# Performance work log

Measured on AMD Instinct MI355X. Metric: run time of the kernel, lower is better.

## Reference

```python
import jax, jax.numpy as jnp
import numpy as np

IGNORE_INDEX = -100


def setup_inputs() -> dict:
    key = jax.random.key(0)
    k1, k2, k3 = jax.random.split(key, 3)
    B, S, D, V = 2, 4096, 2048, 32000
    outputs = jax.random.normal(k1, (B, S, D), dtype=jnp.float32)
    # LM-head weight, nn.Linear convention: [vocab, embed_dim], scaled like typical init
    weight = jax.random.normal(k2, (V, D), dtype=jnp.float32) * (D ** -0.5)
    targets = jax.random.randint(k3, (B, S), 0, V, dtype=jnp.int64)
    return {"outputs": outputs, "weight": weight, "targets": targets}


def reference(outputs, weight, targets):
    # Flatten tokens: [B, S, D] -> [N, D], [B, S] -> [N]
    D = outputs.shape[-1]
    x = outputs.reshape(-1, D)            # [N, D]
    t = targets.reshape(-1)               # [N]
    # Fused linear projection: logits [N, V]
    logits = jnp.einsum("nd,vd->nv", x, weight)
    logp = jax.nn.log_softmax(logits, axis=-1)
    valid = t != IGNORE_INDEX
    safe_t = jnp.where(valid, t, 0)
    # Gather target log-prob per token
    nll = -jnp.take_along_axis(logp, safe_t[:, None], axis=1)[:, 0]  # [N]
    n_valid = jnp.maximum(jnp.sum(valid.astype(nll.dtype)), 1.0)
    loss = jnp.sum(jnp.where(valid, nll, 0.0)) / n_valid
    return loss
```

## Files before the change

kernel.cpp:

```cpp
#include <hip/hip_runtime.h>
#include <hip/hip_bf16.h>
#include <math.h>

#define IGNORE_INDEX (-100)

typedef __attribute__((ext_vector_type(4))) float f32x4;
typedef __attribute__((ext_vector_type(16))) float f32x16;
typedef __attribute__((ext_vector_type(4))) int i32x4;
typedef __attribute__((ext_vector_type(8))) int i32x8;

static const int NTOK = 2 * 4096;
static const int DIM  = 2048;
static const int VOC  = 32000;
static const int BM = 256, BN = 256;
static const int KS = 64;
static const int NPH = DIM / KS;
static const int NVT = VOC / BN;
static const int MT  = NTOK / BM;
static const float WSCALE = 16.0f;
#define SCL1 0x7F7F7F7F


__device__ inline void gload_lds16(const void* g, void* l) {
  __builtin_amdgcn_global_load_lds(
      (const __attribute__((address_space(1))) void*)g,
      (__attribute__((address_space(3))) void*)l,
      16, 0, 0);
}


__global__ void cast_f32_fp8(const float* __restrict__ in,
                             unsigned char* __restrict__ out, long n8, float scale) {
  long i0 = (long)blockIdx.x * blockDim.x + threadIdx.x;
  long stride = (long)gridDim.x * blockDim.x;
  for (long i = i0; i < n8; i += stride) {
    const float4* p = (const float4*)(in + i * 8);
    float4 a = p[0], b = p[1];
    int lo = __builtin_amdgcn_cvt_pk_fp8_f32(a.x * scale, a.y * scale, 0, false);
    lo = __builtin_amdgcn_cvt_pk_fp8_f32(a.z * scale, a.w * scale, lo, true);
    int hi = __builtin_amdgcn_cvt_pk_fp8_f32(b.x * scale, b.y * scale, 0, false);
    hi = __builtin_amdgcn_cvt_pk_fp8_f32(b.z * scale, b.w * scale, hi, true);
    int2 o; o.x = lo; o.y = hi;
    *(int2*)(out + i * 8) = o;
  }
}


#define VM8  asm volatile("s_waitcnt vmcnt(8)" ::: "memory")
#define VM4  asm volatile("s_waitcnt vmcnt(4)" ::: "memory")
#define VM0  asm volatile("s_waitcnt vmcnt(0)" ::: "memory")
#define BARRIER asm volatile("s_barrier" ::: "memory")
#define LGKM0 asm volatile("s_waitcnt lgkmcnt(0)" ::: "memory")

#define MS(ACC, AV, BV) \
  ACC = __builtin_amdgcn_mfma_scale_f32_32x32x64_f8f6f4( \
      AV, BV, ACC, 0, 0, 0, SCL1, 0, SCL1)

#define PACK8(LO, HI) {LO[0], LO[1], LO[2], LO[3], HI[0], HI[1], HI[2], HI[3]}

__launch_bounds__(512, 2)
__global__ void lce_gemm(const unsigned char* __restrict__ xq,
                         const unsigned char* __restrict__ wq,
                         float* __restrict__ pmax, float* __restrict__ psum) {
  extern __shared__ char smem[];
  char* smA = smem;
  char* smB = smem + 65536;

  const int nwg = NVT * MT;
  const int cpx = nwg >> 3;
  const int bid = blockIdx.x;
  const int swz = (bid & 7) * cpx + (bid >> 3);
  const int vt = swz / MT;
  const int mt = swz % MT;
  const int m0 = mt * BM;
  const int v0 = vt * BN;

  const int tid = threadIdx.x;
  const int lane = tid & 63;
  const int w = tid >> 6;
  const int wr = w >> 2, wc = w & 3;
  const int lc = lane & 31;
  const int lh = lane >> 5;

  f32x16 acc[4][2];
#pragma unroll
  for (int i = 0; i < 4; ++i)
#pragma unroll
    for (int j = 0; j < 2; ++j)
#pragma unroll
      for (int r = 0; r < 16; ++r) acc[i][j][r] = 0.f;

  const unsigned char* aS0 = xq + (long)(m0 + w * 32 + lc) * DIM + lh * 32;
  const unsigned char* aS1 = aS0 + 16;
  const unsigned char* bS0 = wq + (long)(v0 + w * 32 + lc) * DIM + lh * 32;
  const unsigned char* bS1 = bS0 + 16;
  char* stA = smA + w * 2048;
  char* stB = smB + w * 2048;

  const char* aRd = smA + wr * 4 * 2048 + lane * 16;
  const char* bRd = smB + wc * 2 * 2048 + lane * 16;

#pragma unroll
  for (int s = 0; s < 3; ++s) {
    gload_lds16(aS0, stA + s * 16384);        aS0 += KS;
    gload_lds16(aS1, stA + s * 16384 + 1024); aS1 += KS;
    gload_lds16(bS0, stB + s * 16384);        bS0 += KS;
    gload_lds16(bS1, stB + s * 16384 + 1024); bS1 += KS;
  }
  VM8;
  BARRIER;

#pragma unroll 1
  for (int n = 0; n < NPH; ++n) {
    const int slot = n & 3;
    const int dst = (n + 3) & 3;
    const char* Ab = aRd + slot * 16384;
    const char* Bb = bRd + slot * 16384;
    const bool stg = (n < NPH - 3);

    i32x4 b0l = *(const i32x4*)(Bb);
    i32x4 b0h = *(const i32x4*)(Bb + 1024);
    i32x4 b1l = *(const i32x4*)(Bb + 2048);
    i32x4 b1h = *(const i32x4*)(Bb + 3072);
    i32x4 a0l = *(const i32x4*)(Ab);
    i32x4 a0h = *(const i32x4*)(Ab + 1024);
    i32x4 a1l = *(const i32x4*)(Ab + 2048);
    i32x4 a1h = *(const i32x4*)(Ab + 3072);
    if (stg) {
      gload_lds16(aS0, stA + dst * 16384);        aS0 += KS;
      gload_lds16(aS1, stA + dst * 16384 + 1024); aS1 += KS;
    }
    BARRIER; LGKM0;
    {
      i32x8 B0 = PACK8(b0l, b0h);
      i32x8 B1 = PACK8(b1l, b1h);
      i32x8 A0 = PACK8(a0l, a0h);
      i32x8 A1 = PACK8(a1l, a1h);
      __builtin_amdgcn_s_setprio(1);
      MS(acc[0][0], A0, B0); MS(acc[0][1], A0, B1);
      MS(acc[1][0], A1, B0); MS(acc[1][1], A1, B1);
      __builtin_amdgcn_s_setprio(0);
    }
    BARRIER;

    i32x4 a2l = *(const i32x4*)(Ab + 4096);
    i32x4 a2h = *(const i32x4*)(Ab + 5120);
    i32x4 a3l = *(const i32x4*)(Ab + 6144);
    i32x4 a3h = *(const i32x4*)(Ab + 7168);
    if (stg) {
      gload_lds16(bS0, stB + dst * 16384);        bS0 += KS;
      gload_lds16(bS1, stB + dst * 16384 + 1024); bS1 += KS;
    }
    BARRIER; LGKM0;
    {
      i32x8 B0 = PACK8(b0l, b0h);
      i32x8 B1 = PACK8(b1l, b1h);
      i32x8 A2 = PACK8(a2l, a2h);
      i32x8 A3 = PACK8(a3l, a3h);
      __builtin_amdgcn_s_setprio(1);
      MS(acc[2][0], A2, B0); MS(acc[2][1], A2, B1);
      MS(acc[3][0], A3, B0); MS(acc[3][1], A3, B1);
      __builtin_amdgcn_s_setprio(0);
    }
    if (n < NPH - 3) { VM8; }
    else if (n == NPH - 3) { VM4; }
    else if (n == NPH - 2) { VM0; }
    BARRIER;
  }

  const float sc = 1.0f / WSCALE;
  float* sm_m = (float*)smem;
  float* sm_s = (float*)(smem + 4096);
  __syncthreads();
#pragma unroll
  for (int i = 0; i < 4; ++i) {
#pragma unroll
    for (int r = 0; r < 16; ++r) {
      float l0 = acc[i][0][r] * sc, l1 = acc[i][1][r] * sc;
      float m = fmaxf(l0, l1);
#pragma unroll
      for (int mk = 1; mk < 32; mk <<= 1) m = fmaxf(m, __shfl_xor(m, mk));
      float s = __expf(l0 - m) + __expf(l1 - m);
#pragma unroll
      for (int mk = 1; mk < 32; mk <<= 1) s += __shfl_xor(s, mk);
      if (lc == 0) {
        int R = wr * 128 + i * 32 + (r & 3) + 8 * (r >> 2) + 4 * lh;
        sm_m[wc * 256 + R] = m;
        sm_s[wc * 256 + R] = s;
      }
    }
  }
  __syncthreads();
  if (tid < BM) {
    float ma = sm_m[tid], mb = sm_m[256 + tid], mc = sm_m[512 + tid], md = sm_m[768 + tid];
    float gm = fmaxf(fmaxf(ma, mb), fmaxf(mc, md));
    float gs = sm_s[tid] * __expf(ma - gm) + sm_s[256 + tid] * __expf(mb - gm) +
               sm_s[512 + tid] * __expf(mc - gm) + sm_s[768 + tid] * __expf(md - gm);
    long row = (long)(m0 + tid);
    pmax[row * NVT + vt] = gm;
    psum[row * NVT + vt] = gs;
  }
}


__global__ void token_reduce(const float* __restrict__ x, const float* __restrict__ wgt,
                             const int* __restrict__ tgt,
                             const float* __restrict__ pmax, const float* __restrict__ psum,
                             float* __restrict__ nll, float* __restrict__ validf) {
  const int n = blockIdx.x;
  const int tid = threadIdx.x;
  const int lane = tid & 63;
  const int w = tid >> 6;
  __shared__ float smr[4];

  const int t = tgt[n];
  const bool valid = (t != IGNORE_INDEX);
  const int ts = valid ? t : 0;

  const float4* xr = (const float4*)(x + (long)n * DIM);
  const float4* wr = (const float4*)(wgt + (long)ts * DIM);
  float d = 0.f;
  for (int i = tid; i < DIM / 4; i += blockDim.x) {
    float4 a = xr[i], b = wr[i];
    d += a.x * b.x + a.y * b.y + a.z * b.z + a.w * b.w;
  }

  float m = (tid < NVT) ? pmax[(long)n * NVT + tid] : -INFINITY;
  float t1 = m;
#pragma unroll
  for (int mk = 1; mk < 64; mk <<= 1) t1 = fmaxf(t1, __shfl_xor(t1, mk));
  if (lane == 0) smr[w] = t1;
  __syncthreads();
  const float gm = fmaxf(fmaxf(smr[0], smr[1]), fmaxf(smr[2], smr[3]));
  __syncthreads();

  float se = (tid < NVT) ? psum[(long)n * NVT + tid] * __expf(m - gm) : 0.f;
#pragma unroll
  for (int mk = 1; mk < 64; mk <<= 1) se += __shfl_xor(se, mk);
  if (lane == 0) smr[w] = se;
  __syncthreads();
  const float gs = smr[0] + smr[1] + smr[2] + smr[3];
  __syncthreads();

#pragma unroll
  for (int mk = 1; mk < 64; mk <<= 1) d += __shfl_xor(d, mk);
  if (lane == 0) smr[w] = d;
  __syncthreads();
  const float gd = smr[0] + smr[1] + smr[2] + smr[3];

  if (tid == 0) {
    nll[n] = valid ? (gm + logf(gs) - gd) : 0.f;
    validf[n] = valid ? 1.f : 0.f;
  }
}


__global__ void final_reduce(const float* __restrict__ nll, const float* __restrict__ validf,
                             float* __restrict__ out, int n) {
  const int tid = threadIdx.x;
  const int lane = tid & 63;
  const int w = tid >> 6;
  __shared__ float sm1[4], sm2[4];
  float s = 0.f, c = 0.f;
  for (int i = tid; i < n; i += blockDim.x) { s += nll[i]; c += validf[i]; }
#pragma unroll
  for (int mk = 1; mk < 64; mk <<= 1) { s += __shfl_xor(s, mk); c += __shfl_xor(c, mk); }
  if (lane == 0) { sm1[w] = s; sm2[w] = c; }
  __syncthreads();
  if (tid == 0) {
    float ts = sm1[0] + sm1[1] + sm1[2] + sm1[3];
    float tc = sm2[0] + sm2[1] + sm2[2] + sm2[3];
    out[0] = ts / fmaxf(tc, 1.0f);
  }
}


extern "C" void kernel_launch(void* const* d_in, const int* in_sizes, int n_in,
                              void* d_out, int out_size, void* d_ws, size_t ws_size,
                              hipStream_t stream) {
  const float* x = (const float*)d_in[0];
  const float* wgt = (const float*)d_in[1];
  const int* tgt = (const int*)d_in[2];
  float* out = (float*)d_out;

  char* ws = (char*)d_ws;
  const size_t xq_off = 0;
  const size_t wq_off = (size_t)NTOK * DIM;
  const size_t pm_off = wq_off + (size_t)VOC * DIM;
  const size_t ps_off = pm_off + (size_t)NTOK * NVT * 4;
  const size_t nl_off = ps_off + (size_t)NTOK * NVT * 4;
  const size_t vf_off = nl_off + (size_t)NTOK * 4;
  const size_t needed = vf_off + (size_t)NTOK * 4;
  if (ws_size < needed) return;

  unsigned char* xq = (unsigned char*)(ws + xq_off);
  unsigned char* wq = (unsigned char*)(ws + wq_off);
  float* pmax = (float*)(ws + pm_off);
  float* psum = (float*)(ws + ps_off);
  float* nllv = (float*)(ws + nl_off);
  float* vldf = (float*)(ws + vf_off);

  cast_f32_fp8<<<2048, 256, 0, stream>>>(x, xq, (long)NTOK * DIM / 8, 1.0f);
  cast_f32_fp8<<<4096, 256, 0, stream>>>(wgt, wq, (long)VOC * DIM / 8, WSCALE);

  (void)hipFuncSetAttribute((const void*)lce_gemm,
                            hipFuncAttributeMaxDynamicSharedMemorySize, 131072);
  lce_gemm<<<NVT * MT, 512, 131072, stream>>>(xq, wq, pmax, psum);

  token_reduce<<<NTOK, 256, 0, stream>>>(x, wgt, tgt, pmax, psum, nllv, vldf);
  final_reduce<<<1, 256, 0, stream>>>(nllv, vldf, out, NTOK);
}
```

Baseline: 1.060 ms.

## Double-buffer LDS fragment registers to overlap reads with MFMA in GEMM main loop

Restructures the FP8 GEMM K-loop so each phase's LDS fragments are read into one register set while MFMAs run on the other (ping-pong), with global->LDS staging issued once per phase. Barriers drop from three per phase to one, and the loop is manually unrolled by two with an explicit epilogue. This raises register pressure (two full A/B fragment sets) at 2 waves/SIMD launch bounds, which risks spills or lower occupancy.

Measured after the change: 1.287 ms. +21.4%, slower.

```diff
diff --git a/kernel.cpp b/kernel.cpp
--- a/kernel.cpp
+++ b/kernel.cpp
@@ -56,7 +56,41 @@
   ACC = __builtin_amdgcn_mfma_scale_f32_32x32x64_f8f6f4( \
       AV, BV, ACC, 0, 0, 0, SCL1, 0, SCL1)
 
-#define PACK8(LO, HI) {LO[0], LO[1], LO[2], LO[3], HI[0], HI[1], HI[2], HI[3]}
+#define STAGE(DST) do { \
+  char* _dA = stA + (DST) * 16384; \
+  char* _dB = stB + (DST) * 16384; \
+  gload_lds16(aS0, _dA); \
+  gload_lds16(aS1, _dA + 1024); \
+  gload_lds16(bS0, _dB); \
+  gload_lds16(bS1, _dB + 1024); \
+  aS0 += KS; aS1 += KS; bS0 += KS; bS1 += KS; \
+} while (0)
+
+#define READS(RING, A0v, A1v, A2v, A3v, B0v, B1v) do { \
+  const char* _Ab = aRd + (RING) * 16384; \
+  const char* _Bb = bRd + (RING) * 16384; \
+  *(i32x4*)&(A0v)         = *(const i32x4*)(_Ab); \
+  *(((i32x4*)&(A0v)) + 1) = *(const i32x4*)(_Ab + 1024); \
+  *(i32x4*)&(A1v)         = *(const i32x4*)(_Ab + 2048); \
+  *(((i32x4*)&(A1v)) + 1) = *(const i32x4*)(_Ab + 3072); \
+  *(i32x4*)&(A2v)         = *(const i32x4*)(_Ab + 4096); \
+  *(((i32x4*)&(A2v)) + 1) = *(const i32x4*)(_Ab + 5120); \
+  *(i32x4*)&(A3v)         = *(const i32x4*)(_Ab + 6144); \
+  *(((i32x4*)&(A3v)) + 1) = *(const i32x4*)(_Ab + 7168); \
+  *(i32x4*)&(B0v)         = *(const i32x4*)(_Bb); \
+  *(((i32x4*)&(B0v)) + 1) = *(const i32x4*)(_Bb + 1024); \
+  *(i32x4*)&(B1v)         = *(const i32x4*)(_Bb + 2048); \
+  *(((i32x4*)&(B1v)) + 1) = *(const i32x4*)(_Bb + 3072); \
+} while (0)
+
+#define MFMA8(A0v, A1v, A2v, A3v, B0v, B1v) do { \
+  __builtin_amdgcn_s_setprio(1); \
+  MS(acc[0][0], A0v, B0v); MS(acc[0][1], A0v, B1v); \
+  MS(acc[1][0], A1v, B0v); MS(acc[1][1], A1v, B1v); \
+  MS(acc[2][0], A2v, B0v); MS(acc[2][1], A2v, B1v); \
+  MS(acc[3][0], A3v, B0v); MS(acc[3][1], A3v, B1v); \
+  __builtin_amdgcn_s_setprio(0); \
+} while (0)
 
 __launch_bounds__(512, 2)
 __global__ void lce_gemm(const unsigned char* __restrict__ xq,
@@ -100,73 +134,41 @@
   const char* aRd = smA + wr * 4 * 2048 + lane * 16;
   const char* bRd = smB + wc * 2 * 2048 + lane * 16;
 
-#pragma unroll
-  for (int s = 0; s < 3; ++s) {
-    gload_lds16(aS0, stA + s * 16384);        aS0 += KS;
-    gload_lds16(aS1, stA + s * 16384 + 1024); aS1 += KS;
-    gload_lds16(bS0, stB + s * 16384);        bS0 += KS;
-    gload_lds16(bS1, stB + s * 16384 + 1024); bS1 += KS;
-  }
+  i32x8 A0a, A1a, A2a, A3a, B0a, B1a;
+  i32x8 A0b, A1b, A2b, A3b, B0b, B1b;
+
+  STAGE(0); STAGE(1); STAGE(2);
   VM8;
   BARRIER;
+  READS(0, A0a, A1a, A2a, A3a, B0a, B1a);
 
 #pragma unroll 1
-  for (int n = 0; n < NPH; ++n) {
-    const int slot = n & 3;
-    const int dst = (n + 3) & 3;
-    const char* Ab = aRd + slot * 16384;
-    const char* Bb = bRd + slot * 16384;
-    const bool stg = (n < NPH - 3);
-
-    i32x4 b0l = *(const i32x4*)(Bb);
-    i32x4 b0h = *(const i32x4*)(Bb + 1024);
-    i32x4 b1l = *(const i32x4*)(Bb + 2048);
-    i32x4 b1h = *(const i32x4*)(Bb + 3072);
-    i32x4 a0l = *(const i32x4*)(Ab);
-    i32x4 a0h = *(const i32x4*)(Ab + 1024);
-    i32x4 a1l = *(const i32x4*)(Ab + 2048);
-    i32x4 a1h = *(const i32x4*)(Ab + 3072);
-    if (stg) {
-      gload_lds16(aS0, stA + dst * 16384);        aS0 += KS;
-      gload_lds16(aS1, stA + dst * 16384 + 1024); aS1 += KS;
-    }
-    BARRIER; LGKM0;
-    {
-      i32x8 B0 = PACK8(b0l, b0h);
-      i32x8 B1 = PACK8(b1l, b1h);
-      i32x8 A0 = PACK8(a0l, a0h);
-      i32x8 A1 = PACK8(a1l, a1h);
-      __builtin_amdgcn_s_setprio(1);
-      MS(acc[0][0], A0, B0); MS(acc[0][1], A0, B1);
-      MS(acc[1][0], A1, B0); MS(acc[1][1], A1, B1);
-      __builtin_amdgcn_s_setprio(0);
-    }
-    BARRIER;
-
-    i32x4 a2l = *(const i32x4*)(Ab + 4096);
-    i32x4 a2h = *(const i32x4*)(Ab + 5120);
-    i32x4 a3l = *(const i32x4*)(Ab + 6144);
-    i32x4 a3h = *(const i32x4*)(Ab + 7168);
-    if (stg) {
-      gload_lds16(bS0, stB + dst * 16384);        bS0 += KS;
-      gload_lds16(bS1, stB + dst * 16384 + 1024); bS1 += KS;
-    }
-    BARRIER; LGKM0;
-    {
-      i32x8 B0 = PACK8(b0l, b0h);
-      i32x8 B1 = PACK8(b1l, b1h);
-      i32x8 A2 = PACK8(a2l, a2h);
-      i32x8 A3 = PACK8(a3l, a3h);
-      __builtin_amdgcn_s_setprio(1);
-      MS(acc[2][0], A2, B0); MS(acc[2][1], A2, B1);
-      MS(acc[3][0], A3, B0); MS(acc[3][1], A3, B1);
-      __builtin_amdgcn_s_setprio(0);
-    }
-    if (n < NPH - 3) { VM8; }
-    else if (n == NPH - 3) { VM4; }
-    else if (n == NPH - 2) { VM0; }
-    BARRIER;
-  }
+  for (int n = 0; n < 28; n += 2) {
+    VM4; BARRIER;
+    STAGE((n + 3) & 3);
+    READS((n + 1) & 3, A0b, A1b, A2b, A3b, B0b, B1b);
+    MFMA8(A0a, A1a, A2a, A3a, B0a, B1a);
+    LGKM0;
+    VM4; BARRIER;
+    STAGE((n + 4) & 3);
+    READS((n + 2) & 3, A0a, A1a, A2a, A3a, B0a, B1a);
+    MFMA8(A0b, A1b, A2b, A3b, B0b, B1b);
+    LGKM0;
+  }
+  VM4; BARRIER;
+  STAGE(3);
+  READS(1, A0b, A1b, A2b, A3b, B0b, B1b);
+  MFMA8(A0a, A1a, A2a, A3a, B0a, B1a);
+  LGKM0;
+  VM4; BARRIER;
+  READS(2, A0a, A1a, A2a, A3a, B0a, B1a);
+  MFMA8(A0b, A1b, A2b, A3b, B0b, B1b);
+  LGKM0;
+  VM0; BARRIER;
+  READS(3, A0b, A1b, A2b, A3b, B0b, B1b);
+  MFMA8(A0a, A1a, A2a, A3a, B0a, B1a);
+  LGKM0;
+  MFMA8(A0b, A1b, A2b, A3b, B0b, B1b);
 
   const float sc = 1.0f / WSCALE;
   float* sm_m = (float*)smem;
```
